# Kernel tuning notes

Hardware: AMD Instinct MI355X
Metric: run time of the kernel (lower is better)

The kernel has to match this reference:

```python
import jax, jax.numpy as jnp
import numpy as np

NUM_AA, EMB, H = 20, 16, 128
IN1 = 1 + 2 + 4 * EMB  # 67: theta, sin/cos phi, 4-residue context
IN2 = 2 + 2 + 4 * EMB  # 68: sin/cos phi_i, sin/cos phi_{i+1}, context


def setup_inputs() -> dict:
    key = jax.random.key(0)
    ks = jax.random.split(key, 12)
    B, L = 64, 4096
    R = jax.random.normal(ks[0], (B, L, 3), dtype=jnp.float32)
    seq = jax.random.randint(ks[1], (B, L), 0, NUM_AA)
    def lin(k, i, o):
        kw, kb = jax.random.split(k)
        s = 1.0 / np.sqrt(i)
        return (jax.random.uniform(kw, (i, o), jnp.float32, -s, s),
                jax.random.uniform(kb, (o,), jnp.float32, -s, s))
    emb = jax.random.normal(ks[2], (NUM_AA, EMB), dtype=jnp.float32)
    tp_W1, tp_b1 = lin(ks[3], IN1, H)
    tp_W2, tp_b2 = lin(ks[4], H, H)
    tp_W3, tp_b3 = lin(ks[5], H, 1)
    pp_W1, pp_b1 = lin(ks[6], IN2, H)
    pp_W2, pp_b2 = lin(ks[7], H, H)
    pp_W3, pp_b3 = lin(ks[8], H, 1)
    return dict(R=R, seq=seq, emb=emb,
                tp_W1=tp_W1, tp_b1=tp_b1, tp_W2=tp_W2, tp_b2=tp_b2, tp_W3=tp_W3, tp_b3=tp_b3,
                pp_W1=pp_W1, pp_b1=pp_b1, pp_W2=pp_W2, pp_b2=pp_b2, pp_W3=pp_W3, pp_b3=pp_b3)


def _mlp(x, W1, b1, W2, b2, W3, b3):
    h = jax.nn.relu(x @ W1 + b1)
    h = jax.nn.relu(h @ W2 + b2)
    return x @ 0.0 if False else h @ W3 + b3


def _bond_angles(R):
    # angle at residue i+1 of triplet (i, i+1, i+2) -> (B, L-2)
    u1 = R[:, :-2] - R[:, 1:-1]
    u2 = R[:, 2:] - R[:, 1:-1]
    c = jnp.cross(u1, u2)
    return jnp.arctan2(jnp.linalg.norm(c, axis=-1), jnp.sum(u1 * u2, axis=-1))


def _torsions(R):
    # dihedral of quadruplet (i..i+3) -> (B, L-3)
    b1 = R[:, 1:-2] - R[:, :-3]
    b2 = R[:, 2:-1] - R[:, 1:-2]
    b3 = R[:, 3:] - R[:, 2:-1]
    n1 = jnp.cross(b1, b2)
    n2 = jnp.cross(b2, b3)
    b2n = b2 / (jnp.linalg.norm(b2, axis=-1, keepdims=True) + 1e-8)
    x = jnp.sum(n1 * n2, axis=-1)
    y = jnp.sum(jnp.cross(n1, n2) * b2n, axis=-1)
    return jnp.arctan2(y, x)


def reference(R, seq, emb,
              tp_W1, tp_b1, tp_W2, tp_b2, tp_W3, tp_b3,
              pp_W1, pp_b1, pp_W2, pp_b2, pp_W3, pp_b3):
    B, L, _ = R.shape
    e = emb[seq]                                   # (B, L, EMB)
    theta = _bond_angles(R)                        # (B, L-2)
    phi = _torsions(R)                             # (B, L-3)
    sc_phi = jnp.stack([jnp.sin(phi), jnp.cos(phi)], axis=-1)  # (B, L-3, 2)
    theta_in = jnp.cos(theta[:, :L - 3])           # use_cos_theta=True
    ctx = jnp.concatenate([e[:, :-3], e[:, 1:-2], e[:, 2:-1], e[:, 3:]], axis=-1)  # (B, L-3, 4*EMB)
    x1 = jnp.concatenate([theta_in[..., None], sc_phi, ctx], axis=-1)  # (B, L-3, 67)
    E1 = _mlp(x1, tp_W1, tp_b1, tp_W2, tp_b2, tp_W3, tp_b3)[..., 0].sum(axis=1)
    x2 = jnp.concatenate([sc_phi[:, :-1], sc_phi[:, 1:], ctx[:, :-1]], axis=-1)    # (B, L-4, 68)
    E2 = _mlp(x2, pp_W1, pp_b1, pp_W2, pp_b2, pp_W3, pp_b3)[..., 0].sum(axis=1)
    return E1 + E2
```

## Files before the change

kernel.cpp:

```cpp
#include <hip/hip_runtime.h>

#define L_   4096
#define LIM0 4093
#define LIM1 4092

typedef short s16x8 __attribute__((ext_vector_type(8)));
typedef float f32x4 __attribute__((ext_vector_type(4)));

__device__ __forceinline__ unsigned int cvt_pk_bf16(float lo, float hi) {
    unsigned int r;
    asm("v_cvt_pk_bf16_f32 %0, %1, %2" : "=v"(r) : "v"(lo), "v"(hi));
    return r;
}

struct F3 { float x, y, z; };
__device__ __forceinline__ F3 ld3(const float* p) { return F3{p[0], p[1], p[2]}; }
__device__ __forceinline__ F3 sub3(F3 a, F3 b) { return F3{a.x-b.x, a.y-b.y, a.z-b.z}; }
__device__ __forceinline__ F3 cross3(F3 a, F3 b) {
    return F3{a.y*b.z - a.z*b.y, a.z*b.x - a.x*b.z, a.x*b.y - a.y*b.x};
}
__device__ __forceinline__ float dot3(F3 a, F3 b) { return a.x*b.x + a.y*b.y + a.z*b.z; }

__device__ __forceinline__ void torsion(F3 a, F3 b, F3 c, F3 d, float& sn, float& cs) {
    F3 v1 = sub3(b, a), v2 = sub3(c, b), v3 = sub3(d, c);
    F3 n1 = cross3(v1, v2), n2 = cross3(v2, v3);
    float x = dot3(n1, n2);
    F3 m = cross3(n1, n2);
    float bn = sqrtf(dot3(v2, v2)) + 1e-8f;
    float y = dot3(m, v2) / bn;
    float inv = rsqrtf(x*x + y*y + 1e-30f);
    sn = y * inv; cs = x * inv;
}

#define MFMA16 __builtin_amdgcn_mfma_f32_16x16x32_bf16

__device__ __forceinline__ void xstore(unsigned short* S, int rr, int c, unsigned short v) {
    S[rr*128 + (((c >> 3) ^ (rr & 15)) << 3) + (c & 7)] = v;
}

__global__ __launch_bounds__(256) void ss_pre(
    const float* __restrict__ R, uint2* __restrict__ featG,
    const float* __restrict__ emb, uint4* __restrict__ embbfG,
    const float* __restrict__ tpW1, const float* __restrict__ tpb1,
    const float* __restrict__ tpW2,
    const float* __restrict__ ppW1, const float* __restrict__ ppb1,
    const float* __restrict__ ppW2,
    uint4* __restrict__ wfragG) {
    const int t = threadIdx.x;
    if (blockIdx.x == 16) {
        if (blockIdx.y >= 28) return;
        if (blockIdx.y == 0 && t < 40) {
            const float* ep = emb + (t >> 1) * 16 + (t & 1) * 8;
            embbfG[t] = make_uint4(cvt_pk_bf16(ep[0], ep[1]), cvt_pk_bf16(ep[2], ep[3]),
                                   cvt_pk_bf16(ep[4], ep[5]), cvt_pk_bf16(ep[6], ep[7]));
        }
        const int F = blockIdx.y * 256 + t;
        int l = F & 63, q = F >> 6;
        int kkL = q % 7; q /= 7;
        int mt = q & 1; q >>= 1;
        int w = q & 3, mode = q >> 2;
        int g = l >> 4, ln = l & 15;
        int hc = w*32 + mt*16 + ln;
        const float* W1  = mode ? ppW1 : tpW1;
        const float* Bi1 = mode ? ppb1 : tpb1;
        const float* W2  = mode ? ppW2 : tpW2;
        float v[8];
        #pragma unroll
        for (int j = 0; j < 8; j++) {
            if (kkL < 3) {
                int c = kkL*32 + g*8 + j;
                int kp;
                if (mode) kp = (c < 64) ? c + 4 : ((c < 68) ? c - 64 : ((c == 68) ? -2 : -1));
                else      kp = (c < 64) ? c + 3 : ((c == 64) ? 0 : ((c == 65) ? -2 :
                               ((c == 66) ? 1 : ((c == 67) ? 2 : -1))));
                v[j] = (kp == -1) ? 0.f : ((kp == -2) ? Bi1[hc] : W1[kp*128 + hc]);
            } else {
                v[j] = W2[((kkL - 3)*32 + g*8 + j)*128 + hc];
            }
        }
        wfragG[F] = make_uint4(cvt_pk_bf16(v[0], v[1]), cvt_pk_bf16(v[2], v[3]),
                               cvt_pk_bf16(v[4], v[5]), cvt_pk_bf16(v[6], v[7]));
        return;
    }
    const int p = blockIdx.x * 256 + t;
    const int b = blockIdx.y;
    if (p >= LIM0) return;
    const float* Rp = R + ((size_t)(b * L_ + p)) * 3;
    F3 p0 = ld3(Rp), p1 = ld3(Rp + 3), p2 = ld3(Rp + 6), p3 = ld3(Rp + 9);
    F3 u1 = sub3(p0, p1), u2 = sub3(p2, p1);
    F3 cr = cross3(u1, u2);
    float d = dot3(u1, u2);
    float ct = d * rsqrtf(d * d + dot3(cr, cr) + 1e-30f);
    float sp, cp; torsion(p0, p1, p2, p3, sp, cp);
    featG[(size_t)b * L_ + p] = make_uint2(cvt_pk_bf16(ct, 1.0f), cvt_pk_bf16(sp, cp));
}

__global__ __launch_bounds__(256) void ss_mlp(
    const int* __restrict__ seq, const uint2* __restrict__ featG,
    const uint4* __restrict__ embbfG, const uint4* __restrict__ wfragG,
    const float* __restrict__ tpb2, const float* __restrict__ ppb2,
    float* __restrict__ ws) {

    __shared__ __align__(16) unsigned short Xs[64*128];
    __shared__ __align__(16) unsigned short H1s[64*128];

    const int b = blockIdx.y, mode = blockIdx.z, bx = blockIdx.x;
    const int lim = mode ? LIM1 : LIM0;
    const float* Bi2 = mode ? ppb2 : tpb2;

    const int t = threadIdx.x;
    const int w = t >> 6, l = t & 63, g = l >> 4, ln = l & 15;
    const int g2 = g >> 1, gh = g & 1;
    const int r = t >> 2, sub = t & 3;
    const int rw = r & 15;
    const size_t bL = (size_t)b * L_;

    int aa0, aa_n1; uint2 fv0 = {}, fv0b = {}, fvn = {}, fvnb = {};
    {
        const int p0 = min(bx * 64 + r, lim - 1);
        aa0 = seq[bL + p0 + sub];
        const int p1 = min(bx * 64 + 512 + r, lim - 1);
        aa_n1 = seq[bL + p1 + sub];
        if (sub == 0) {
            fv0 = featG[bL + p0];
            if (mode) fv0b = featG[bL + p0 + 1];
        }
    }

    for (int i = t; i < 1024; i += 256) ((uint4*)Xs)[i] = make_uint4(0u, 0u, 0u, 0u);

    s16x8 fr[2][7];
    {
        const uint4* wf = wfragG + (size_t)(mode*4 + w) * (2*7*64);
        #pragma unroll
        for (int mt = 0; mt < 2; mt++)
            #pragma unroll
            for (int kkL = 0; kkL < 7; kkL++)
                fr[mt][kkL] = *(const s16x8*)(wf + (mt*7 + kkL)*64 + l);
    }
    float bb2[2][4];
    #pragma unroll
    for (int mt = 0; mt < 2; mt++)
        #pragma unroll
        for (int i = 0; i < 4; i++)
            bb2[mt][i] = Bi2[w*32 + mt*16 + g*4 + i];

    uint4 e0_ = embbfG[aa0*2], e1_ = embbfG[aa0*2 + 1];

    __syncthreads();

    *(uint4*)(Xs + r*128 + (((sub*2    ) ^ rw) << 3)) = e0_;
    *(uint4*)(Xs + r*128 + (((sub*2 + 1) ^ rw) << 3)) = e1_;
    if (sub == 0) {
        uint2 u = mode ? make_uint2(fv0.y, fv0b.y) : fv0;
        *(uint2*)(Xs + r*128 + ((8 ^ rw) << 3)) = u;
    }
    if (t < 64) xstore(Xs, t, 68, (unsigned short)0x3F80);
    __syncthreads();

    float s[2][4] = {{0.f,0.f,0.f,0.f},{0.f,0.f,0.f,0.f}};

    for (int it = 0; it < 8; it++) {
        const int pos0 = (bx + it*8) << 6;

        uint4 e0n, e1n;
        if (it < 7) {
            e0n = embbfG[aa_n1*2]; e1n = embbfG[aa_n1*2 + 1];
            const int p1 = min(pos0 + 512 + r, lim - 1);
            if (sub == 0) {
                fvn = featG[bL + p1];
                if (mode) fvnb = featG[bL + p1 + 1];
            }
        }
        int aa_n2;
        if (it < 6) aa_n2 = seq[bL + min(pos0 + 1024 + r, lim - 1) + sub];

        #pragma unroll
        for (int pt = 0; pt < 4; pt++) {
            const int row = pt*16 + ln;
            const unsigned short* base = Xs + row*128;
            f32x4 c0 = {0.f,0.f,0.f,0.f}, c1 = {0.f,0.f,0.f,0.f};
            #pragma unroll
            for (int kk = 0; kk < 3; kk++) {
                s16x8 bf = *(const s16x8*)(base + (((kk*4 + g) ^ ln) << 3));
                c0 = MFMA16(fr[0][kk], bf, c0, 0, 0, 0);
                c1 = MFMA16(fr[1][kk], bf, c1, 0, 0, 0);
            }
            unsigned short* hb = H1s + row*128;
            uint2 u;
            u.x = cvt_pk_bf16(fmaxf(c0[0], 0.f), fmaxf(c0[1], 0.f));
            u.y = cvt_pk_bf16(fmaxf(c0[2], 0.f), fmaxf(c0[3], 0.f));
            *(uint2*)(hb + (((w*4 + g2) ^ ln) << 3) + gh*4) = u;
            u.x = cvt_pk_bf16(fmaxf(c1[0], 0.f), fmaxf(c1[1], 0.f));
            u.y = cvt_pk_bf16(fmaxf(c1[2], 0.f), fmaxf(c1[3], 0.f));
            *(uint2*)(hb + (((w*4 + 2 + g2) ^ ln) << 3) + gh*4) = u;
        }
        __syncthreads();

        if (it < 7) {
            *(uint4*)(Xs + r*128 + (((sub*2    ) ^ rw) << 3)) = e0n;
            *(uint4*)(Xs + r*128 + (((sub*2 + 1) ^ rw) << 3)) = e1n;
            if (sub == 0) {
                uint2 u = mode ? make_uint2(fvn.y, fvnb.y) : fvn;
                *(uint2*)(Xs + r*128 + ((8 ^ rw) << 3)) = u;
            }
        }

        #pragma unroll
        for (int pt = 0; pt < 4; pt++) {
            const int row = pt*16 + ln;
            const unsigned short* hbase = H1s + row*128;
            f32x4 d0 = {0.f,0.f,0.f,0.f}, d1 = {0.f,0.f,0.f,0.f};
            #pragma unroll
            for (int kk = 0; kk < 4; kk++) {
                s16x8 bf = *(const s16x8*)(hbase + (((kk*4 + g) ^ ln) << 3));
                d0 = MFMA16(fr[0][3+kk], bf, d0, 0, 0, 0);
                d1 = MFMA16(fr[1][3+kk], bf, d1, 0, 0, 0);
            }
            if (pos0 + row < lim) {
                #pragma unroll
                for (int i = 0; i < 4; i++) {
                    s[0][i] += fmaxf(d0[i] + bb2[0][i], 0.f);
                    s[1][i] += fmaxf(d1[i] + bb2[1][i], 0.f);
                }
            }
        }
        __syncthreads();

        if (it < 6) aa_n1 = aa_n2;
    }

    #pragma unroll
    for (int mt = 0; mt < 2; mt++)
        #pragma unroll
        for (int i = 0; i < 4; i++) {
            float v = s[mt][i];
            v += __shfl_xor(v, 1, 64); v += __shfl_xor(v, 2, 64);
            v += __shfl_xor(v, 4, 64); v += __shfl_xor(v, 8, 64);
            if (ln == 0)
                atomicAdd(ws + ((b*2 + mode) << 7) + w*32 + mt*16 + g*4 + i, v);
        }
}

__global__ void ss_finish(const float* __restrict__ ws,
                          const float* __restrict__ tpW3, const float* __restrict__ tpb3,
                          const float* __restrict__ ppW3, const float* __restrict__ ppb3,
                          float* __restrict__ out) {
    const int b = blockIdx.x, t = threadIdx.x;
    float v = ws[(b*2 + 0)*128 + t] * tpW3[t] + ws[(b*2 + 1)*128 + t] * ppW3[t];
    #pragma unroll
    for (int off = 1; off < 64; off <<= 1) v += __shfl_xor(v, off, 64);
    __shared__ float ps[2];
    if ((t & 63) == 0) ps[t >> 6] = v;
    __syncthreads();
    if (t == 0) out[b] = ps[0] + ps[1] + 4093.f * tpb3[0] + 4092.f * ppb3[0];
}

extern "C" void kernel_launch(void* const* d_in, const int* in_sizes, int n_in,
                              void* d_out, int out_size, void* d_ws, size_t ws_size,
                              hipStream_t stream) {
    (void)in_sizes; (void)n_in; (void)out_size; (void)ws_size;
    const float* R    = (const float*)d_in[0];
    const int*   seq  = (const int*)d_in[1];
    const float* emb  = (const float*)d_in[2];
    const float* tpW1 = (const float*)d_in[3];
    const float* tpb1 = (const float*)d_in[4];
    const float* tpW2 = (const float*)d_in[5];
    const float* tpb2 = (const float*)d_in[6];
    const float* tpW3 = (const float*)d_in[7];
    const float* tpb3 = (const float*)d_in[8];
    const float* ppW1 = (const float*)d_in[9];
    const float* ppb1 = (const float*)d_in[10];
    const float* ppW2 = (const float*)d_in[11];
    const float* ppb2 = (const float*)d_in[12];
    const float* ppW3 = (const float*)d_in[13];
    const float* ppb3 = (const float*)d_in[14];

    char* wsb = (char*)d_ws;
    float* ws     = (float*)wsb;
    uint2* featG  = (uint2*)(wsb + (64<<10));
    uint4* embbfG = (uint4*)(wsb + (64<<10) + (2<<20));
    uint4* wfragG = (uint4*)(wsb + (64<<10) + (2<<20) + 1024);

    hipMemsetAsync(ws, 0, 64*2*128*sizeof(float), stream);
    ss_pre<<<dim3(17, 64), 256, 0, stream>>>(R, featG, emb, embbfG,
                                             tpW1, tpb1, tpW2, ppW1, ppb1, ppW2, wfragG);
    ss_mlp<<<dim3(8, 64, 2), 256, 0, stream>>>(seq, featG, embbfG, wfragG,
                                               tpb2, ppb2, ws);
    ss_finish<<<64, 128, 0, stream>>>(ws, tpW3, tpb3, ppW3, ppb3, (float*)d_out);
}
```

Before: 47.54 us.

## Fuse geometric feature computation into MLP kernel via shared-memory staging

The per-residue bond-angle and torsion features are now computed inside the MLP kernel into a shared-memory buffer, instead of by a separate pre-pass that wrote them to global memory. Each block now owns a contiguous 512-residue span rather than an interleaved one. The pre-kernel is reduced to weight and embedding packing with a tiny grid. This removes a global round-trip and a large launch, but the two MLP modes (the z grid dimension) now compute the same features twice.

```diff
diff --git a/kernel.cpp b/kernel.cpp
--- a/kernel.cpp
+++ b/kernel.cpp
@@ -38,8 +38,7 @@
     S[rr*128 + (((c >> 3) ^ (rr & 15)) << 3) + (c & 7)] = v;
 }
 
-__global__ __launch_bounds__(256) void ss_pre(
-    const float* __restrict__ R, uint2* __restrict__ featG,
+__global__ __launch_bounds__(256) void ss_prew(
     const float* __restrict__ emb, uint4* __restrict__ embbfG,
     const float* __restrict__ tpW1, const float* __restrict__ tpb1,
     const float* __restrict__ tpW2,
@@ -47,62 +46,48 @@
     const float* __restrict__ ppW2,
     uint4* __restrict__ wfragG) {
     const int t = threadIdx.x;
-    if (blockIdx.x == 16) {
-        if (blockIdx.y >= 28) return;
-        if (blockIdx.y == 0 && t < 40) {
-            const float* ep = emb + (t >> 1) * 16 + (t & 1) * 8;
-            embbfG[t] = make_uint4(cvt_pk_bf16(ep[0], ep[1]), cvt_pk_bf16(ep[2], ep[3]),
-                                   cvt_pk_bf16(ep[4], ep[5]), cvt_pk_bf16(ep[6], ep[7]));
-        }
-        const int F = blockIdx.y * 256 + t;
-        int l = F & 63, q = F >> 6;
-        int kkL = q % 7; q /= 7;
-        int mt = q & 1; q >>= 1;
-        int w = q & 3, mode = q >> 2;
-        int g = l >> 4, ln = l & 15;
-        int hc = w*32 + mt*16 + ln;
-        const float* W1  = mode ? ppW1 : tpW1;
-        const float* Bi1 = mode ? ppb1 : tpb1;
-        const float* W2  = mode ? ppW2 : tpW2;
-        float v[8];
-        #pragma unroll
-        for (int j = 0; j < 8; j++) {
-            if (kkL < 3) {
-                int c = kkL*32 + g*8 + j;
-                int kp;
-                if (mode) kp = (c < 64) ? c + 4 : ((c < 68) ? c - 64 : ((c == 68) ? -2 : -1));
-                else      kp = (c < 64) ? c + 3 : ((c == 64) ? 0 : ((c == 65) ? -2 :
-                               ((c == 66) ? 1 : ((c == 67) ? 2 : -1))));
-                v[j] = (kp == -1) ? 0.f : ((kp == -2) ? Bi1[hc] : W1[kp*128 + hc]);
-            } else {
-                v[j] = W2[((kkL - 3)*32 + g*8 + j)*128 + hc];
-            }
-        }
-        wfragG[F] = make_uint4(cvt_pk_bf16(v[0], v[1]), cvt_pk_bf16(v[2], v[3]),
-                               cvt_pk_bf16(v[4], v[5]), cvt_pk_bf16(v[6], v[7]));
-        return;
-    }
-    const int p = blockIdx.x * 256 + t;
-    const int b = blockIdx.y;
-    if (p >= LIM0) return;
-    const float* Rp = R + ((size_t)(b * L_ + p)) * 3;
-    F3 p0 = ld3(Rp), p1 = ld3(Rp + 3), p2 = ld3(Rp + 6), p3 = ld3(Rp + 9);
-    F3 u1 = sub3(p0, p1), u2 = sub3(p2, p1);
-    F3 cr = cross3(u1, u2);
-    float d = dot3(u1, u2);
-    float ct = d * rsqrtf(d * d + dot3(cr, cr) + 1e-30f);
-    float sp, cp; torsion(p0, p1, p2, p3, sp, cp);
-    featG[(size_t)b * L_ + p] = make_uint2(cvt_pk_bf16(ct, 1.0f), cvt_pk_bf16(sp, cp));
+    if (blockIdx.x == 0 && t < 40) {
+        const float* ep = emb + (t >> 1) * 16 + (t & 1) * 8;
+        embbfG[t] = make_uint4(cvt_pk_bf16(ep[0], ep[1]), cvt_pk_bf16(ep[2], ep[3]),
+                               cvt_pk_bf16(ep[4], ep[5]), cvt_pk_bf16(ep[6], ep[7]));
+    }
+    const int F = blockIdx.x * 256 + t;
+    int l = F & 63, q = F >> 6;
+    int kkL = q % 7; q /= 7;
+    int mt = q & 1; q >>= 1;
+    int w = q & 3, mode = q >> 2;
+    int g = l >> 4, ln = l & 15;
+    int hc = w*32 + mt*16 + ln;
+    const float* W1  = mode ? ppW1 : tpW1;
+    const float* Bi1 = mode ? ppb1 : tpb1;
+    const float* W2  = mode ? ppW2 : tpW2;
+    float v[8];
+    #pragma unroll
+    for (int j = 0; j < 8; j++) {
+        if (kkL < 3) {
+            int c = kkL*32 + g*8 + j;
+            int kp;
+            if (mode) kp = (c < 64) ? c + 4 : ((c < 68) ? c - 64 : ((c == 68) ? -2 : -1));
+            else      kp = (c < 64) ? c + 3 : ((c == 64) ? 0 : ((c == 65) ? -2 :
+                           ((c == 66) ? 1 : ((c == 67) ? 2 : -1))));
+            v[j] = (kp == -1) ? 0.f : ((kp == -2) ? Bi1[hc] : W1[kp*128 + hc]);
+        } else {
+            v[j] = W2[((kkL - 3)*32 + g*8 + j)*128 + hc];
+        }
+    }
+    wfragG[F] = make_uint4(cvt_pk_bf16(v[0], v[1]), cvt_pk_bf16(v[2], v[3]),
+                           cvt_pk_bf16(v[4], v[5]), cvt_pk_bf16(v[6], v[7]));
 }
 
 __global__ __launch_bounds__(256) void ss_mlp(
-    const int* __restrict__ seq, const uint2* __restrict__ featG,
+    const float* __restrict__ R, const int* __restrict__ seq,
     const uint4* __restrict__ embbfG, const uint4* __restrict__ wfragG,
     const float* __restrict__ tpb2, const float* __restrict__ ppb2,
     float* __restrict__ ws) {
 
     __shared__ __align__(16) unsigned short Xs[64*128];
     __shared__ __align__(16) unsigned short H1s[64*128];
+    __shared__ __align__(8) uint2 featL[513];
 
     const int b = blockIdx.y, mode = blockIdx.z, bx = blockIdx.x;
     const int lim = mode ? LIM1 : LIM0;
@@ -114,17 +99,37 @@
     const int r = t >> 2, sub = t & 3;
     const int rw = r & 15;
     const size_t bL = (size_t)b * L_;
-
-    int aa0, aa_n1; uint2 fv0 = {}, fv0b = {}, fvn = {}, fvnb = {};
+    const int base = bx * 512;
+
+    #pragma unroll
+    for (int rep = 0; rep < 2; rep++) {
+        const int i = t + rep*256;
+        const int pe = min(base + i, LIM0 - 1);
+        const float* Rp = R + ((size_t)(bL + pe)) * 3;
+        F3 p0 = ld3(Rp), p1 = ld3(Rp+3), p2 = ld3(Rp+6), p3 = ld3(Rp+9);
+        F3 u1 = sub3(p0, p1), u2 = sub3(p2, p1);
+        F3 cr = cross3(u1, u2);
+        float d = dot3(u1, u2);
+        float ct = d * rsqrtf(d*d + dot3(cr, cr) + 1e-30f);
+        float sp, cp; torsion(p0, p1, p2, p3, sp, cp);
+        featL[i] = make_uint2(cvt_pk_bf16(ct, 1.0f), cvt_pk_bf16(sp, cp));
+    }
+    if (t == 0) {
+        const int pe = min(base + 512, LIM0 - 1);
+        const float* Rp = R + ((size_t)(bL + pe)) * 3;
+        F3 p0 = ld3(Rp), p1 = ld3(Rp+3), p2 = ld3(Rp+6), p3 = ld3(Rp+9);
+        F3 u1 = sub3(p0, p1), u2 = sub3(p2, p1);
+        F3 cr = cross3(u1, u2);
+        float d = dot3(u1, u2);
+        float ct = d * rsqrtf(d*d + dot3(cr, cr) + 1e-30f);
+        float sp, cp; torsion(p0, p1, p2, p3, sp, cp);
+        featL[512] = make_uint2(cvt_pk_bf16(ct, 1.0f), cvt_pk_bf16(sp, cp));
+    }
+
+    int aa0, aa_n1;
     {
-        const int p0 = min(bx * 64 + r, lim - 1);
-        aa0 = seq[bL + p0 + sub];
-        const int p1 = min(bx * 64 + 512 + r, lim - 1);
-        aa_n1 = seq[bL + p1 + sub];
-        if (sub == 0) {
-            fv0 = featG[bL + p0];
-            if (mode) fv0b = featG[bL + p0 + 1];
-        }
+        aa0  = seq[bL + min(base + r,      lim - 1) + sub];
+        aa_n1 = seq[bL + min(base + 64 + r, lim - 1) + sub];
     }
 
     for (int i = t; i < 1024; i += 256) ((uint4*)Xs)[i] = make_uint4(0u, 0u, 0u, 0u);
@@ -152,7 +157,9 @@
     *(uint4*)(Xs + r*128 + (((sub*2    ) ^ rw) << 3)) = e0_;
     *(uint4*)(Xs + r*128 + (((sub*2 + 1) ^ rw) << 3)) = e1_;
     if (sub == 0) {
-        uint2 u = mode ? make_uint2(fv0.y, fv0b.y) : fv0;
+        const int i0 = min(base + r, lim - 1) - base;
+        uint2 f0 = featL[i0];
+        uint2 u = mode ? make_uint2(f0.y, featL[i0 + 1].y) : f0;
         *(uint2*)(Xs + r*128 + ((8 ^ rw) << 3)) = u;
     }
     if (t < 64) xstore(Xs, t, 68, (unsigned short)0x3F80);
@@ -161,28 +168,21 @@
     float s[2][4] = {{0.f,0.f,0.f,0.f},{0.f,0.f,0.f,0.f}};
 
     for (int it = 0; it < 8; it++) {
-        const int pos0 = (bx + it*8) << 6;
+        const int pos0 = base + it*64;
 
         uint4 e0n, e1n;
-        if (it < 7) {
-            e0n = embbfG[aa_n1*2]; e1n = embbfG[aa_n1*2 + 1];
-            const int p1 = min(pos0 + 512 + r, lim - 1);
-            if (sub == 0) {
-                fvn = featG[bL + p1];
-                if (mode) fvnb = featG[bL + p1 + 1];
-            }
-        }
+        if (it < 7) { e0n = embbfG[aa_n1*2]; e1n = embbfG[aa_n1*2 + 1]; }
         int aa_n2;
-        if (it < 6) aa_n2 = seq[bL + min(pos0 + 1024 + r, lim - 1) + sub];
+        if (it < 6) aa_n2 = seq[bL + min(pos0 + 128 + r, lim - 1) + sub];
 
         #pragma unroll
         for (int pt = 0; pt < 4; pt++) {
             const int row = pt*16 + ln;
-            const unsigned short* base = Xs + row*128;
+            const unsigned short* bse = Xs + row*128;
             f32x4 c0 = {0.f,0.f,0.f,0.f}, c1 = {0.f,0.f,0.f,0.f};
             #pragma unroll
             for (int kk = 0; kk < 3; kk++) {
-                s16x8 bf = *(const s16x8*)(base + (((kk*4 + g) ^ ln) << 3));
+                s16x8 bf = *(const s16x8*)(bse + (((kk*4 + g) ^ ln) << 3));
                 c0 = MFMA16(fr[0][kk], bf, c0, 0, 0, 0);
                 c1 = MFMA16(fr[1][kk], bf, c1, 0, 0, 0);
             }
@@ -201,7 +201,9 @@
             *(uint4*)(Xs + r*128 + (((sub*2    ) ^ rw) << 3)) = e0n;
             *(uint4*)(Xs + r*128 + (((sub*2 + 1) ^ rw) << 3)) = e1n;
             if (sub == 0) {
-                uint2 u = mode ? make_uint2(fvn.y, fvnb.y) : fvn;
+                const int i1 = min(pos0 + 64 + r, lim - 1) - base;
+                uint2 f0 = featL[i1];
+                uint2 u = mode ? make_uint2(f0.y, featL[i1 + 1].y) : f0;
                 *(uint2*)(Xs + r*128 + ((8 ^ rw) << 3)) = u;
             }
         }
@@ -278,14 +280,13 @@
 
     char* wsb = (char*)d_ws;
     float* ws     = (float*)wsb;
-    uint2* featG  = (uint2*)(wsb + (64<<10));
-    uint4* embbfG = (uint4*)(wsb + (64<<10) + (2<<20));
-    uint4* wfragG = (uint4*)(wsb + (64<<10) + (2<<20) + 1024);
+    uint4* embbfG = (uint4*)(wsb + (64<<10));
+    uint4* wfragG = (uint4*)(wsb + (64<<10) + 1024);
 
     hipMemsetAsync(ws, 0, 64*2*128*sizeof(float), stream);
-    ss_pre<<<dim3(17, 64), 256, 0, stream>>>(R, featG, emb, embbfG,
-                                             tpW1, tpb1, tpW2, ppW1, ppb1, ppW2, wfragG);
-    ss_mlp<<<dim3(8, 64, 2), 256, 0, stream>>>(seq, featG, embbfG, wfragG,
+    ss_prew<<<28, 256, 0, stream>>>(emb, embbfG,
+                                    tpW1, tpb1, tpW2, ppW1, ppb1, ppW2, wfragG);
+    ss_mlp<<<dim3(8, 64, 2), 256, 0, stream>>>(R, seq, embbfG, wfragG,
                                                tpb2, ppb2, ws);
     ss_finish<<<64, 128, 0, stream>>>(ws, tpW3, tpb3, ppW3, ppb3, (float*)d_out);
 }
```

After: 49.03 us. 3.1% more time.
